# Performance work log

Measured on AMD Instinct MI355X. Metric: run time of the kernel, lower is better.

Reference implementation:

```python
import jax, jax.numpy as jnp
import numpy as np

N = 131072   # octree nodes at this depth
K = 27       # 3x3x3 kernel taps
CIN = 32
COUT = 32
EPS = 1e-5   # BatchNorm1d default eps


def setup_inputs() -> dict:
    key = jax.random.key(0)
    k1, k2, k3, k4, k5 = jax.random.split(key, 5)
    data = jax.random.normal(k1, (N, CIN), dtype=jnp.float32)
    # deconv weight: one [Cin, Cout] matrix per kernel tap
    weight = jax.random.normal(k2, (K, CIN, COUT), dtype=jnp.float32) * 0.05
    gamma = 1.0 + 0.1 * jax.random.normal(k3, (COUT,), dtype=jnp.float32)
    beta = 0.1 * jax.random.normal(k4, (COUT,), dtype=jnp.float32)
    # octree neighbor table: for each input node, the K output nodes it scatters into
    neigh = jax.random.randint(k5, (N, K), 0, N, dtype=jnp.int32)
    return {"data": data, "weight": weight, "gamma": gamma, "beta": beta, "neigh": neigh}


def reference(data, weight, gamma, beta, neigh):
    # Sparse transposed conv (stride=1): each node i produces a contribution
    # data[i] @ weight[k] that is scatter-added into output node neigh[i, k].
    contrib = jnp.einsum('ni,kio->nko', data, weight)          # [N, K, Cout]
    out = jax.ops.segment_sum(contrib.reshape(-1, COUT),
                              neigh.reshape(-1),
                              num_segments=N)                   # [N, Cout]
    # BatchNorm1d (training mode: batch statistics over the node dimension)
    mean = jnp.mean(out, axis=0)
    var = jnp.var(out, axis=0)
    y = gamma * (out - mean) * jax.lax.rsqrt(var + EPS) + beta
    # ReLU
    return jnp.maximum(y, 0.0)
```

## Files before the change

kernel.cpp:

```cpp
#include <hip/hip_runtime.h>
#include <hip/hip_bf16.h>
#include <hip/hip_fp16.h>

#define NN 131072
#define KK 27
#define CC 32
#define EPSV 1e-5f

#define WS_STATS 0
#define WS_WPERM 256
#define WS_ACC   65536
#define WS_NEEDED ((size_t)WS_ACC + (size_t)NN * CC * 2)

typedef __bf16 bf16x8 __attribute__((ext_vector_type(8)));
typedef short s16x8 __attribute__((ext_vector_type(8)));
typedef float f32x4 __attribute__((ext_vector_type(4)));

__device__ inline unsigned short f2bf(float f) {
    unsigned int u = __float_as_uint(f);
    u += 0x7FFF + ((u >> 16) & 1);
    return (unsigned short)(u >> 16);
}

__global__ __launch_bounds__(256) void prep_weights_kernel(
    const float* __restrict__ weight, unsigned short* __restrict__ wperm)
{
    const int p = blockIdx.x * 256 + threadIdx.x;
    if (p >= KK * 1024) return;
    const int k  = p >> 10;
    const int ci = (p >> 5) & 31;
    const int c  = p & 31;
    const unsigned short v = f2bf(weight[p]);
    const int chalf = c & 1;
    const int col   = c >> 1;
    const int fl = col | ((ci >> 3) << 4);
    const int j = ci & 7;
    wperm[(((k << 1) | chalf) * 64 + fl) * 8 + j] = v;
}

__global__ __launch_bounds__(256) void scatter_kernel(
    const float* __restrict__ data, const unsigned short* __restrict__ wperm,
    const int* __restrict__ neigh, __half2* __restrict__ acc2)
{
    const int tid = threadIdx.x;
    const int lane = tid & 63;
    const int wv = tid >> 6;
    const int node_base = blockIdx.x * 128 + wv * 32;

    const int quad = lane >> 4;
    const int m = lane & 15;
    const int rq = quad << 2;

    s16x8 afr[2];
    #pragma unroll
    for (int g = 0; g < 2; ++g) {
        const int node = node_base + g * 16 + m;
        const float* src = data + node * 32 + quad * 8;
        const float4 v0 = *(const float4*)(src);
        const float4 v1 = *(const float4*)(src + 4);
        s16x8 s;
        s[0] = (short)f2bf(v0.x); s[1] = (short)f2bf(v0.y);
        s[2] = (short)f2bf(v0.z); s[3] = (short)f2bf(v0.w);
        s[4] = (short)f2bf(v1.x); s[5] = (short)f2bf(v1.y);
        s[6] = (short)f2bf(v1.z); s[7] = (short)f2bf(v1.w);
        afr[g] = s;
    }

    const s16x8* wp = (const s16x8*)wperm;
    const f32x4 zero = {0.f, 0.f, 0.f, 0.f};

    int nj0[4], nj1[4];
    #pragma unroll
    for (int r = 0; r < 4; ++r) {
        nj0[r] = neigh[(node_base + rq + r) * KK];
        nj1[r] = neigh[(node_base + 16 + rq + r) * KK];
    }
    s16x8 bs0 = wp[lane];
    s16x8 bs1 = wp[64 + lane];

    for (int k = 0; k < KK; ++k) {
        const int kn = (k < KK - 1) ? k + 1 : k;
        int nn0[4], nn1[4];
        #pragma unroll
        for (int r = 0; r < 4; ++r) {
            nn0[r] = neigh[(node_base + rq + r) * KK + kn];
            nn1[r] = neigh[(node_base + 16 + rq + r) * KK + kn];
        }
        const s16x8 nbs0 = wp[(kn * 2) * 64 + lane];
        const s16x8 nbs1 = wp[(kn * 2 + 1) * 64 + lane];

        {
            const f32x4 d0 = __builtin_amdgcn_mfma_f32_16x16x32_bf16(
                __builtin_bit_cast(bf16x8, afr[0]), __builtin_bit_cast(bf16x8, bs0),
                zero, 0, 0, 0);
            const f32x4 d1 = __builtin_amdgcn_mfma_f32_16x16x32_bf16(
                __builtin_bit_cast(bf16x8, afr[0]), __builtin_bit_cast(bf16x8, bs1),
                zero, 0, 0, 0);
            #pragma unroll
            for (int r = 0; r < 4; ++r) {
                __half2 v;
                v.x = __float2half(d0[r]);
                v.y = __float2half(d1[r]);
                unsafeAtomicAdd(&acc2[nj0[r] * 16 + m], v);
            }
        }
        {
            const f32x4 d0 = __builtin_amdgcn_mfma_f32_16x16x32_bf16(
                __builtin_bit_cast(bf16x8, afr[1]), __builtin_bit_cast(bf16x8, bs0),
                zero, 0, 0, 0);
            const f32x4 d1 = __builtin_amdgcn_mfma_f32_16x16x32_bf16(
                __builtin_bit_cast(bf16x8, afr[1]), __builtin_bit_cast(bf16x8, bs1),
                zero, 0, 0, 0);
            #pragma unroll
            for (int r = 0; r < 4; ++r) {
                __half2 v;
                v.x = __float2half(d0[r]);
                v.y = __float2half(d1[r]);
                unsafeAtomicAdd(&acc2[nj1[r] * 16 + m], v);
            }
        }

        bs0 = nbs0; bs1 = nbs1;
        #pragma unroll
        for (int r = 0; r < 4; ++r) { nj0[r] = nn0[r]; nj1[r] = nn1[r]; }
    }
}

__global__ __launch_bounds__(256) void stats_kernel(
    const __half2* __restrict__ acc2, float* __restrict__ stats)
{
    __shared__ float ls[16][33], ls2[16][33];
    const int tid = threadIdx.x;
    const int c2 = tid & 15, rg = tid >> 4;
    float sx = 0.f, sy = 0.f, s2x = 0.f, s2y = 0.f;
    const int row0 = blockIdx.x * 512;
    for (int it = 0; it < 32; ++it) {
        const __half2 h = acc2[(row0 + it * 16 + rg) * 16 + c2];
        const float vx = __half2float(h.x), vy = __half2float(h.y);
        sx += vx; sy += vy; s2x += vx * vx; s2y += vy * vy;
    }
    ls[rg][2 * c2] = sx;  ls[rg][2 * c2 + 1] = sy;
    ls2[rg][2 * c2] = s2x; ls2[rg][2 * c2 + 1] = s2y;
    __syncthreads();
    if (tid < 32) {
        float S = 0.f, S2 = 0.f;
        #pragma unroll
        for (int g = 0; g < 16; ++g) { S += ls[g][tid]; S2 += ls2[g][tid]; }
        atomicAdd(&stats[tid], S);
        atomicAdd(&stats[32 + tid], S2);
    }
}

__global__ __launch_bounds__(256) void bn_relu_kernel(
    const __half2* __restrict__ acc2, float* __restrict__ out,
    const float* __restrict__ stats,
    const float* __restrict__ gamma, const float* __restrict__ beta)
{
    __shared__ float sc[32], sh[32];
    const int tid = threadIdx.x;
    if (tid < 32) {
        const float mean = stats[tid] * (1.0f / NN);
        const float var  = stats[32 + tid] * (1.0f / NN) - mean * mean;
        const float s = gamma[tid] * rsqrtf(var + EPSV);
        sc[tid] = s;
        sh[tid] = beta[tid] - mean * s;
    }
    __syncthreads();
    const int idx = blockIdx.x * 256 + tid;
    const int c0 = (idx & 3) << 3;
    const __half2 h4[4] = { acc2[idx * 4], acc2[idx * 4 + 1],
                            acc2[idx * 4 + 2], acc2[idx * 4 + 3] };
    float4 o0, o1;
    o0.x = fmaxf(__half2float(h4[0].x) * sc[c0]     + sh[c0],     0.f);
    o0.y = fmaxf(__half2float(h4[0].y) * sc[c0 + 1] + sh[c0 + 1], 0.f);
    o0.z = fmaxf(__half2float(h4[1].x) * sc[c0 + 2] + sh[c0 + 2], 0.f);
    o0.w = fmaxf(__half2float(h4[1].y) * sc[c0 + 3] + sh[c0 + 3], 0.f);
    o1.x = fmaxf(__half2float(h4[2].x) * sc[c0 + 4] + sh[c0 + 4], 0.f);
    o1.y = fmaxf(__half2float(h4[2].y) * sc[c0 + 5] + sh[c0 + 5], 0.f);
    o1.z = fmaxf(__half2float(h4[3].x) * sc[c0 + 6] + sh[c0 + 6], 0.f);
    o1.w = fmaxf(__half2float(h4[3].y) * sc[c0 + 7] + sh[c0 + 7], 0.f);
    ((float4*)out)[idx * 2]     = o0;
    ((float4*)out)[idx * 2 + 1] = o1;
}

__global__ __launch_bounds__(256) void scatter_f32_kernel(
    const float* __restrict__ data, const float* __restrict__ weight,
    const int* __restrict__ neigh, float* __restrict__ out)
{
    __shared__ unsigned short wfrag[KK * 2 * 64 * 8];
    const int tid = threadIdx.x;
    const int lane = tid & 63;
    const int wv = tid >> 6;
    const int node_base = blockIdx.x * 128;
    for (int p = tid; p < KK * 1024; p += 256) {
        const int k  = p >> 10;
        const int ci = (p >> 5) & 31;
        const int c  = p & 31;
        const unsigned short v = f2bf(weight[p]);
        const int chalf = c >> 4;
        const int fl = (c & 15) | ((ci >> 3) << 4);
        const int j = ci & 7;
        wfrag[(((k << 1) | chalf) * 64 + fl) * 8 + j] = v;
    }
    const int quad = lane >> 4;
    const int m = lane & 15;
    s16x8 afr[2];
    #pragma unroll
    for (int g = 0; g < 2; ++g) {
        const int node = node_base + wv * 32 + g * 16 + m;
        const float* src = data + node * 32 + quad * 8;
        const float4 v0 = *(const float4*)(src);
        const float4 v1 = *(const float4*)(src + 4);
        s16x8 s;
        s[0] = (short)f2bf(v0.x); s[1] = (short)f2bf(v0.y);
        s[2] = (short)f2bf(v0.z); s[3] = (short)f2bf(v0.w);
        s[4] = (short)f2bf(v1.x); s[5] = (short)f2bf(v1.y);
        s[6] = (short)f2bf(v1.z); s[7] = (short)f2bf(v1.w);
        afr[g] = s;
    }
    __syncthreads();
    const int rq = quad << 2;
    const f32x4 zero = {0.f, 0.f, 0.f, 0.f};
    for (int k = 0; k < KK; ++k) {
        int nj[2][4];
        #pragma unroll
        for (int g = 0; g < 2; ++g)
            #pragma unroll
            for (int r = 0; r < 4; ++r) {
                const int node = node_base + wv * 32 + g * 16 + rq + r;
                nj[g][r] = neigh[node * KK + k];
            }
        #pragma unroll
        for (int ch = 0; ch < 2; ++ch) {
            const s16x8 bs = *(const s16x8*)&wfrag[((((k << 1) | ch)) * 64 + lane) * 8];
            const bf16x8 bfr = __builtin_bit_cast(bf16x8, bs);
            const int c = (ch << 4) | m;
            #pragma unroll
            for (int g = 0; g < 2; ++g) {
                f32x4 a2 = __builtin_amdgcn_mfma_f32_16x16x32_bf16(
                    __builtin_bit_cast(bf16x8, afr[g]), bfr, zero, 0, 0, 0);
                #pragma unroll
                for (int r = 0; r < 4; ++r)
                    __hip_atomic_fetch_add(&out[nj[g][r] * 32 + c], a2[r],
                                           __ATOMIC_RELAXED, __HIP_MEMORY_SCOPE_AGENT);
            }
        }
    }
}

__global__ __launch_bounds__(256) void stats_f32_kernel(
    const float* __restrict__ out, float* __restrict__ stats)
{
    __shared__ float ls[256], ls2[256];
    const int tid = threadIdx.x;
    const int c = tid & 31, rg = tid >> 5;
    float s = 0.f, s2 = 0.f;
    const int row0 = blockIdx.x * 512;
    for (int it = 0; it < 64; ++it) {
        const float v = out[(row0 + it * 8 + rg) * 32 + c];
        s += v; s2 += v * v;
    }
    ls[tid] = s; ls2[tid] = s2;
    __syncthreads();
    if (tid < 32) {
        float S = 0.f, S2 = 0.f;
        #pragma unroll
        for (int r = 0; r < 8; ++r) { S += ls[r * 32 + tid]; S2 += ls2[r * 32 + tid]; }
        atomicAdd(&stats[tid], S);
        atomicAdd(&stats[32 + tid], S2);
    }
}

__global__ __launch_bounds__(256) void bn_relu_f32_kernel(
    float* __restrict__ out, const float* __restrict__ stats,
    const float* __restrict__ gamma, const float* __restrict__ beta)
{
    __shared__ float sc[32], sh[32];
    const int tid = threadIdx.x;
    if (tid < 32) {
        const float mean = stats[tid] * (1.0f / NN);
        const float var  = stats[32 + tid] * (1.0f / NN) - mean * mean;
        const float s = gamma[tid] * rsqrtf(var + EPSV);
        sc[tid] = s;
        sh[tid] = beta[tid] - mean * s;
    }
    __syncthreads();
    const int idx = blockIdx.x * 256 + tid;
    float4 v = ((float4*)out)[idx];
    const int cb = (idx & 7) << 2;
    v.x = fmaxf(v.x * sc[cb]     + sh[cb],     0.f);
    v.y = fmaxf(v.y * sc[cb + 1] + sh[cb + 1], 0.f);
    v.z = fmaxf(v.z * sc[cb + 2] + sh[cb + 2], 0.f);
    v.w = fmaxf(v.w * sc[cb + 3] + sh[cb + 3], 0.f);
    ((float4*)out)[idx] = v;
}

extern "C" void kernel_launch(void* const* d_in, const int* in_sizes, int n_in,
                              void* d_out, int out_size, void* d_ws, size_t ws_size,
                              hipStream_t stream) {
    const float* data   = (const float*)d_in[0];
    const float* weight = (const float*)d_in[1];
    const float* gamma  = (const float*)d_in[2];
    const float* beta   = (const float*)d_in[3];
    const int*   neigh  = (const int*)d_in[4];
    float* out = (float*)d_out;
    char* ws = (char*)d_ws;
    float* stats = (float*)(ws + WS_STATS);

    if (ws_size >= WS_NEEDED) {
        __half2* acc2 = (__half2*)(ws + WS_ACC);
        unsigned short* wperm = (unsigned short*)(ws + WS_WPERM);
        hipMemsetAsync(ws + WS_STATS, 0, 256, stream);
        hipMemsetAsync(ws + WS_ACC, 0, (size_t)NN * CC * 2, stream);
        prep_weights_kernel<<<(KK * 1024 + 255) / 256, 256, 0, stream>>>(weight, wperm);
        scatter_kernel<<<NN / 128, 256, 0, stream>>>(data, wperm, neigh, acc2);
        stats_kernel<<<NN / 512, 256, 0, stream>>>(acc2, stats);
        bn_relu_kernel<<<(NN * CC / 8) / 256, 256, 0, stream>>>(acc2, out, stats, gamma, beta);
    } else {
        hipMemsetAsync(out, 0, (size_t)NN * CC * sizeof(float), stream);
        hipMemsetAsync(stats, 0, 64 * sizeof(float), stream);
        scatter_f32_kernel<<<NN / 128, 256, 0, stream>>>(data, weight, neigh, out);
        stats_f32_kernel<<<NN / 512, 256, 0, stream>>>(out, stats);
        bn_relu_f32_kernel<<<(NN * CC / 4) / 256, 256, 0, stream>>>(out, stats, gamma, beta);
    }
}
```

Baseline: 271.4 us.

## Replace atomic scatter with bucketed inverse-index gather and fused BN statistics

Builds an inverse neighbour table by bucketing every (input node, tap) pair per output node with a counter, capped at 64 slots. Each output row then gathers fp16 input rows, pre-sums them per tap in LDS, and runs one fp16 MFMA chain over the 27 taps. The output is written once in fp32, and the batch-norm sums are reduced in the same kernel. This replaces tens of millions of half2 atomics on the output with a few million integer atomics on counters. In exchange it adds a pair-fill pass, fp16 accumulation of the per-tap sums, silent truncation of rows with more than 64 contributors, and a much larger workspace requirement.

Result: slower. 544.9 us (+100.8%).

```diff
diff --git a/kernel.cpp b/kernel.cpp
--- a/kernel.cpp
+++ b/kernel.cpp
@@ -7,12 +7,22 @@
 #define CC 32
 #define EPSV 1e-5f
 
-#define WS_STATS 0
-#define WS_WPERM 256
-#define WS_ACC   65536
-#define WS_NEEDED ((size_t)WS_ACC + (size_t)NN * CC * 2)
+#define WS_STATS   0
+#define WS_CNT     256
+#define WS_WPERM   (256 + 524288)
+#define WS_PAIRS   579840
+#define WS_DATA16  34134272
+#define WS_NEED_GATHER ((size_t)WS_DATA16 + (size_t)NN * CC * 2)
+
+#define T2_WPERM 256
+#define T2_ACC   65536
+#define WS_NEED_T2 ((size_t)T2_ACC + (size_t)NN * CC * 2)
+
+#define CAP  64
+#define XSTR 472
 
 typedef __bf16 bf16x8 __attribute__((ext_vector_type(8)));
+typedef _Float16 f16x8 __attribute__((ext_vector_type(8)));
 typedef short s16x8 __attribute__((ext_vector_type(8)));
 typedef float f32x4 __attribute__((ext_vector_type(4)));
 
@@ -21,8 +31,186 @@
     u += 0x7FFF + ((u >> 16) & 1);
     return (unsigned short)(u >> 16);
 }
-
-__global__ __launch_bounds__(256) void prep_weights_kernel(
+__device__ inline unsigned short f2h(float f) {
+    return __builtin_bit_cast(unsigned short, __float2half(f));
+}
+__device__ inline unsigned int h2add(unsigned int a, unsigned int b) {
+    __half2 x = __builtin_bit_cast(__half2, a);
+    __half2 y = __builtin_bit_cast(__half2, b);
+    return __builtin_bit_cast(unsigned int, __hadd2(x, y));
+}
+
+
+__global__ __launch_bounds__(256) void prep_kernel(
+    const float* __restrict__ data, const float* __restrict__ weight,
+    unsigned short* __restrict__ data16, unsigned short* __restrict__ wperm)
+{
+    const int b = blockIdx.x;
+    if (b < 2048) {
+        const int tg = b * 256 + threadIdx.x;
+        const float4 v0 = ((const float4*)data)[tg * 2];
+        const float4 v1 = ((const float4*)data)[tg * 2 + 1];
+        union { unsigned short us[8]; uint4 u4; } o;
+        o.us[0] = f2h(v0.x); o.us[1] = f2h(v0.y);
+        o.us[2] = f2h(v0.z); o.us[3] = f2h(v0.w);
+        o.us[4] = f2h(v1.x); o.us[5] = f2h(v1.y);
+        o.us[6] = f2h(v1.z); o.us[7] = f2h(v1.w);
+        ((uint4*)data16)[tg] = o.u4;
+    } else {
+        const int p = (b - 2048) * 256 + threadIdx.x;
+        const int k  = p >> 10;
+        const int ci = (p >> 5) & 31;
+        const int c  = p & 31;
+        const unsigned short v = f2h(weight[p]);
+        const int chalf = c & 1;
+        const int col   = c >> 1;
+        const int fl = col | ((ci >> 3) << 4);
+        const int j = ci & 7;
+        wperm[(((k << 1) | chalf) * 64 + fl) * 8 + j] = v;
+    }
+}
+
+__global__ __launch_bounds__(256) void fill_kernel(
+    const int* __restrict__ neigh, unsigned int* __restrict__ cnt,
+    unsigned int* __restrict__ pairs)
+{
+    const unsigned int p = blockIdx.x * 256 + threadIdx.x;
+    const unsigned int o = (unsigned int)neigh[p];
+    const unsigned int i = p / 27u;
+    const unsigned int k = p - i * 27u;
+    const unsigned int slot = atomicAdd(&cnt[o], 1u);
+    if (slot < CAP) pairs[(o << 6) | slot] = (i << 5) | k;
+}
+
+__global__ __launch_bounds__(256) void gather_kernel(
+    const unsigned short* __restrict__ data16,
+    const unsigned short* __restrict__ wperm,
+    const unsigned int* __restrict__ cnt, const unsigned int* __restrict__ pairs,
+    float* __restrict__ out, float* __restrict__ stats)
+{
+    __shared__ unsigned short Xs[4][16 * XSTR];
+    __shared__ float sarr[4][16][4];
+
+    const int tid = threadIdx.x;
+    const int lane = tid & 63;
+    const int wv = tid >> 6;
+    const int row0 = blockIdx.x * 64 + wv * 16;
+
+    const int rl  = lane >> 2;
+    const int seg = lane & 3;
+    const int row_g = row0 + rl;
+
+    const unsigned int cfull = cnt[row_g];
+    const int c = (int)(cfull < (unsigned)CAP ? cfull : (unsigned)CAP);
+    const int cm1 = c > 0 ? c - 1 : 0;
+    int maxc = c;
+    #pragma unroll
+    for (int off = 1; off < 64; off <<= 1) {
+        const int o2 = __shfl_xor(maxc, off);
+        maxc = maxc > o2 ? maxc : o2;
+    }
+
+    const unsigned int* prow = pairs + ((size_t)row_g << 6);
+
+    const int quad = lane >> 4;
+    const int m = lane & 15;
+    f32x4 acc0 = {0.f, 0.f, 0.f, 0.f}, acc1 = {0.f, 0.f, 0.f, 0.f};
+    const uint4* wq = (const uint4*)wperm;
+    const uint4* dq = (const uint4*)data16;
+    unsigned short* xw = &Xs[wv][0];
+
+    for (int g = 0; g < 2; ++g) {
+        const int k0 = g * 14;
+        const int NT = g ? 13 : 14;
+
+        {
+            const uint4 z = {0u, 0u, 0u, 0u};
+            #pragma unroll
+            for (int it = 0; it < 15; ++it) {
+                const int idx = lane + it * 64;
+                if (idx < (16 * XSTR) / 8) ((uint4*)xw)[idx] = z;
+            }
+        }
+
+        unsigned int p0 = prow[0];
+        unsigned int p1 = prow[1 < cm1 ? 1 : cm1];
+        unsigned int p2 = prow[2 < cm1 ? 2 : cm1];
+        unsigned int p3 = prow[3 < cm1 ? 3 : cm1];
+        uint4 d0 = {0,0,0,0}, d1 = {0,0,0,0};
+        {
+            const int kk = (int)(p0 & 31u) - k0;
+            if (kk >= 0 && kk < NT) d0 = dq[(((p0 >> 5) & (NN - 1)) << 2) | seg];
+        }
+        {
+            const int kk = (int)(p1 & 31u) - k0;
+            if (kk >= 0 && kk < NT) d1 = dq[(((p1 >> 5) & (NN - 1)) << 2) | seg];
+        }
+
+        for (int t = 0; t < maxc; ++t) {
+            const int tp = t + 4;
+            const unsigned int pn = prow[tp < cm1 ? tp : cm1];
+            uint4 dn = {0,0,0,0};
+            {
+                const int kk = (int)(p2 & 31u) - k0;
+                if (kk >= 0 && kk < NT) dn = dq[(((p2 >> 5) & (NN - 1)) << 2) | seg];
+            }
+            {
+                const int kk = (int)(p0 & 31u) - k0;
+                if (t < c && kk >= 0 && kk < NT) {
+                    uint4* xp = (uint4*)(xw + rl * XSTR + kk * 32 + seg * 8);
+                    uint4 cur = *xp;
+                    cur.x = h2add(cur.x, d0.x); cur.y = h2add(cur.y, d0.y);
+                    cur.z = h2add(cur.z, d0.z); cur.w = h2add(cur.w, d0.w);
+                    *xp = cur;
+                }
+            }
+            p0 = p1; p1 = p2; p2 = p3; p3 = pn;
+            d0 = d1; d1 = dn;
+        }
+
+        uint4 b0 = wq[(k0 * 2 + 0) * 64 + lane];
+        uint4 b1 = wq[(k0 * 2 + 1) * 64 + lane];
+        for (int kk = 0; kk < NT; ++kk) {
+            const int ktn = (kk + 1 < NT) ? (k0 + kk + 1) : (k0 + kk);
+            const uint4 nb0 = wq[(ktn * 2 + 0) * 64 + lane];
+            const uint4 nb1 = wq[(ktn * 2 + 1) * 64 + lane];
+            const uint4 av = *(const uint4*)(xw + m * XSTR + kk * 32 + quad * 8);
+            const f16x8 af = __builtin_bit_cast(f16x8, av);
+            acc0 = __builtin_amdgcn_mfma_f32_16x16x32_f16(
+                af, __builtin_bit_cast(f16x8, b0), acc0, 0, 0, 0);
+            acc1 = __builtin_amdgcn_mfma_f32_16x16x32_f16(
+                af, __builtin_bit_cast(f16x8, b1), acc1, 0, 0, 0);
+            b0 = nb0; b1 = nb1;
+        }
+    }
+
+    float s0 = 0.f, s1 = 0.f, q0 = 0.f, q1 = 0.f;
+    #pragma unroll
+    for (int r = 0; r < 4; ++r) {
+        const float a = acc0[r], b = acc1[r];
+        s0 += a; s1 += b; q0 += a * a; q1 += b * b;
+        float2 v; v.x = a; v.y = b;
+        *(float2*)(out + ((size_t)(row0 + quad * 4 + r)) * 32 + 2 * m) = v;
+    }
+    s0 += __shfl_xor(s0, 16); s0 += __shfl_xor(s0, 32);
+    s1 += __shfl_xor(s1, 16); s1 += __shfl_xor(s1, 32);
+    q0 += __shfl_xor(q0, 16); q0 += __shfl_xor(q0, 32);
+    q1 += __shfl_xor(q1, 16); q1 += __shfl_xor(q1, 32);
+    if (quad == 0) {
+        sarr[wv][m][0] = s0; sarr[wv][m][1] = s1;
+        sarr[wv][m][2] = q0; sarr[wv][m][3] = q1;
+    }
+    __syncthreads();
+    if (tid < 64) {
+        const int ch = tid & 31, isq = tid >> 5;
+        float v = 0.f;
+        #pragma unroll
+        for (int w = 0; w < 4; ++w) v += sarr[w][ch >> 1][(isq << 1) | (ch & 1)];
+        atomicAdd(&stats[isq * 32 + ch], v);
+    }
+}
+
+__global__ __launch_bounds__(256) void prep_weights_bf16_kernel(
     const float* __restrict__ weight, unsigned short* __restrict__ wperm)
 {
     const int p = blockIdx.x * 256 + threadIdx.x;
@@ -46,7 +234,6 @@
     const int lane = tid & 63;
     const int wv = tid >> 6;
     const int node_base = blockIdx.x * 128 + wv * 32;
-
     const int quad = lane >> 4;
     const int m = lane & 15;
     const int rq = quad << 2;
@@ -88,7 +275,6 @@
         }
         const s16x8 nbs0 = wp[(kn * 2) * 64 + lane];
         const s16x8 nbs1 = wp[(kn * 2 + 1) * 64 + lane];
-
         {
             const f32x4 d0 = __builtin_amdgcn_mfma_f32_16x16x32_bf16(
                 __builtin_bit_cast(bf16x8, afr[0]), __builtin_bit_cast(bf16x8, bs0),
@@ -119,7 +305,6 @@
                 unsafeAtomicAdd(&acc2[nj1[r] * 16 + m], v);
             }
         }
-
         bs0 = nbs0; bs1 = nbs1;
         #pragma unroll
         for (int r = 0; r < 4; ++r) { nj0[r] = nn0[r]; nj1[r] = nn1[r]; }
@@ -307,18 +492,28 @@
     char* ws = (char*)d_ws;
     float* stats = (float*)(ws + WS_STATS);
 
-    if (ws_size >= WS_NEEDED) {
-        __half2* acc2 = (__half2*)(ws + WS_ACC);
-        unsigned short* wperm = (unsigned short*)(ws + WS_WPERM);
+    if (ws_size >= WS_NEED_GATHER) {
+        unsigned int*   cnt    = (unsigned int*)(ws + WS_CNT);
+        unsigned short* wperm  = (unsigned short*)(ws + WS_WPERM);
+        unsigned int*   pairs  = (unsigned int*)(ws + WS_PAIRS);
+        unsigned short* data16 = (unsigned short*)(ws + WS_DATA16);
+        hipMemsetAsync(ws, 0, 256 + (size_t)NN * 4, stream);
+        prep_kernel<<<2156, 256, 0, stream>>>(data, weight, data16, wperm);
+        fill_kernel<<<(NN * KK) / 256, 256, 0, stream>>>(neigh, cnt, pairs);
+        gather_kernel<<<NN / 64, 256, 0, stream>>>(data16, wperm, cnt, pairs, out, stats);
+        bn_relu_f32_kernel<<<(NN * CC / 4) / 256, 256, 0, stream>>>(out, stats, gamma, beta);
+    } else if (ws_size >= WS_NEED_T2) {
+        __half2* acc2 = (__half2*)(ws + T2_ACC);
+        unsigned short* wperm = (unsigned short*)(ws + T2_WPERM);
         hipMemsetAsync(ws + WS_STATS, 0, 256, stream);
-        hipMemsetAsync(ws + WS_ACC, 0, (size_t)NN * CC * 2, stream);
-        prep_weights_kernel<<<(KK * 1024 + 255) / 256, 256, 0, stream>>>(weight, wperm);
+        hipMemsetAsync(ws + T2_ACC, 0, (size_t)NN * CC * 2, stream);
+        prep_weights_bf16_kernel<<<(KK * 1024 + 255) / 256, 256, 0, stream>>>(weight, wperm);
         scatter_kernel<<<NN / 128, 256, 0, stream>>>(data, wperm, neigh, acc2);
         stats_kernel<<<NN / 512, 256, 0, stream>>>(acc2, stats);
         bn_relu_kernel<<<(NN * CC / 8) / 256, 256, 0, stream>>>(acc2, out, stats, gamma, beta);
     } else {
         hipMemsetAsync(out, 0, (size_t)NN * CC * sizeof(float), stream);
-        hipMemsetAsync(stats, 0, 64 * sizeof(float), stream);
+        hipMemsetAsync(ws + WS_STATS, 0, 64 * sizeof(float), stream);
         scatter_f32_kernel<<<NN / 128, 256, 0, stream>>>(data, weight, neigh, out);
         stats_f32_kernel<<<NN / 512, 256, 0, stream>>>(out, stats);
         bn_relu_f32_kernel<<<(NN * CC / 4) / 256, 256, 0, stream>>>(out, stats, gamma, beta);
```

## Replace global atomic scatter with bin-sorted gather matmul and LDS accumulation

Applied to the files above, without the earlier changes.

Adds a new default path that turns the scatter into a gather. The (node, tap) records are partitioned into 512 bins by destination node, then counting-sorted by tap within each bin. A per-bin kernel runs fp16 MFMA on the gathered input rows and accumulates results with shared-memory float atomics. That kernel also writes fp32 outputs directly and fuses the BatchNorm statistics reduction. The aim is to remove the global fp16 atomics and the separate stats pass, at the cost of extra passes over the neighbor table. Bin capacity is fixed, so a skewed index distribution would silently drop contributions.

Result: slower. 729.7 us (+168.9%).

```diff
diff --git a/kernel.cpp b/kernel.cpp
--- a/kernel.cpp
+++ b/kernel.cpp
@@ -7,12 +7,24 @@
 #define CC 32
 #define EPSV 1e-5f
 
-#define WS_STATS 0
-#define WS_WPERM 256
-#define WS_ACC   65536
-#define WS_NEEDED ((size_t)WS_ACC + (size_t)NN * CC * 2)
+#define NBINS   512
+#define CAPBIN  7680
+#define CAPB    24
+#define WS_STATS   0
+#define WS_GCNT    256
+#define WS_KOFF    2304
+#define WS_WPERM   59648
+#define WS_RAW     114944
+#define WS_SORT    15843584
+#define WS_DATA16  31572224
+#define WS_NEED_GATHER ((size_t)WS_DATA16 + (size_t)NN * CC * 2)
+
+#define T2_WPERM 256
+#define T2_ACC   65536
+#define WS_NEED_T2 ((size_t)T2_ACC + (size_t)NN * CC * 2)
 
 typedef __bf16 bf16x8 __attribute__((ext_vector_type(8)));
+typedef _Float16 f16x8 __attribute__((ext_vector_type(8)));
 typedef short s16x8 __attribute__((ext_vector_type(8)));
 typedef float f32x4 __attribute__((ext_vector_type(4)));
 
@@ -21,8 +33,229 @@
     u += 0x7FFF + ((u >> 16) & 1);
     return (unsigned short)(u >> 16);
 }
-
-__global__ __launch_bounds__(256) void prep_weights_kernel(
+__device__ inline unsigned short f2h(float f) {
+    return __builtin_bit_cast(unsigned short, __float2half(f));
+}
+
+
+__global__ __launch_bounds__(256) void prep_kernel(
+    const float* __restrict__ data, const float* __restrict__ weight,
+    unsigned short* __restrict__ data16, unsigned short* __restrict__ wperm)
+{
+    const int b = blockIdx.x;
+    if (b < 2048) {
+        const int tg = b * 256 + threadIdx.x;
+        const float4 v0 = ((const float4*)data)[tg * 2];
+        const float4 v1 = ((const float4*)data)[tg * 2 + 1];
+        union { unsigned short us[8]; uint4 u4; } o;
+        o.us[0] = f2h(v0.x); o.us[1] = f2h(v0.y);
+        o.us[2] = f2h(v0.z); o.us[3] = f2h(v0.w);
+        o.us[4] = f2h(v1.x); o.us[5] = f2h(v1.y);
+        o.us[6] = f2h(v1.z); o.us[7] = f2h(v1.w);
+        ((uint4*)data16)[tg] = o.u4;
+    } else {
+        const int p = (b - 2048) * 256 + threadIdx.x;
+        const int k  = p >> 10;
+        const int ci = (p >> 5) & 31;
+        const int c  = p & 31;
+        const unsigned short v = f2h(weight[p]);
+        const int chalf = c & 1;
+        const int col   = c >> 1;
+        const int fl = col | ((ci >> 3) << 4);
+        const int j = ci & 7;
+        wperm[(((k << 1) | chalf) * 64 + fl) * 8 + j] = v;
+    }
+}
+
+__global__ __launch_bounds__(256) void partition_kernel(
+    const int* __restrict__ neigh, unsigned int* __restrict__ gcnt,
+    unsigned int* __restrict__ raw)
+{
+    __shared__ unsigned int lcnt[NBINS];
+    __shared__ unsigned int lbuf[NBINS * CAPB];
+    const int tid = threadIdx.x;
+    for (int t = tid; t < NBINS; t += 256) lcnt[t] = 0;
+    __syncthreads();
+    const int base = blockIdx.x * 4096;
+    #pragma unroll
+    for (int j = 0; j < 16; ++j) {
+        const int p = base + j * 256 + tid;
+        const unsigned int o = (unsigned int)neigh[p];
+        const unsigned int i = (unsigned int)p / 27u;
+        const unsigned int k = (unsigned int)p - i * 27u;
+        const unsigned int rec = (k << 25) | (i << 8) | (o & 255u);
+        const unsigned int bin = o >> 8;
+        const unsigned int slot = atomicAdd(&lcnt[bin], 1u);
+        if (slot < CAPB) {
+            lbuf[bin * CAPB + slot] = rec;
+        } else {
+            const unsigned int gp = atomicAdd(&gcnt[bin], 1u);
+            if (gp < CAPBIN) raw[(size_t)bin * CAPBIN + gp] = rec;
+        }
+    }
+    __syncthreads();
+    for (int b2 = tid; b2 < NBINS; b2 += 256) {
+        unsigned int nb = lcnt[b2]; if (nb > CAPB) nb = CAPB;
+        if (nb == 0) continue;
+        const unsigned int gbase = atomicAdd(&gcnt[b2], nb);
+        for (unsigned int s = 0; s < nb; ++s) {
+            const unsigned int gp = gbase + s;
+            if (gp < CAPBIN) raw[(size_t)b2 * CAPBIN + gp] = lbuf[b2 * CAPB + s];
+        }
+    }
+}
+
+__global__ __launch_bounds__(256) void binsort_kernel(
+    const unsigned int* __restrict__ gcnt, const unsigned int* __restrict__ raw,
+    unsigned int* __restrict__ sorted, unsigned int* __restrict__ koff)
+{
+    __shared__ unsigned int hist[28];
+    __shared__ unsigned int woffs[27];
+    const int b = blockIdx.x, tid = threadIdx.x;
+    if (tid < 28) hist[tid] = 0;
+    __syncthreads();
+    unsigned int n = gcnt[b]; if (n > CAPBIN) n = CAPBIN;
+    const unsigned int* rp = raw + (size_t)b * CAPBIN;
+    for (unsigned int t = tid; t < n; t += 256)
+        atomicAdd(&hist[rp[t] >> 25], 1u);
+    __syncthreads();
+    if (tid == 0) {
+        unsigned int run = 0;
+        for (int j = 0; j < 27; ++j) {
+            const unsigned int h = hist[j];
+            hist[j] = run; woffs[j] = run; run += h;
+        }
+        hist[27] = run;
+    }
+    __syncthreads();
+    if (tid < 28) koff[b * 28 + tid] = hist[tid];
+    unsigned int* sp = sorted + (size_t)b * CAPBIN;
+    for (unsigned int t = tid; t < n; t += 256) {
+        const unsigned int r = rp[t];
+        const unsigned int pos = atomicAdd(&woffs[r >> 25], 1u);
+        sp[pos] = r & 0x01FFFFFFu;
+    }
+}
+
+__global__ __launch_bounds__(256) void gathermm_kernel(
+    const unsigned short* __restrict__ data16,
+    const unsigned short* __restrict__ wperm,
+    const unsigned int* __restrict__ sorted,
+    const unsigned int* __restrict__ koff,
+    float* __restrict__ out, float* __restrict__ stats)
+{
+    __shared__ float accS[256 * 33];
+    __shared__ float ps[8][32], ps2[8][32];
+    const int tid = threadIdx.x;
+    const int lane = tid & 63, wv = tid >> 6;
+    const int b = blockIdx.x;
+
+    for (int t = tid; t < 256 * 33; t += 256) accS[t] = 0.f;
+    __syncthreads();
+
+    const int q = lane >> 4, m = lane & 15;
+    const uint4* wq = (const uint4*)wperm;
+    const uint4* dq = (const uint4*)data16;
+    const unsigned int* so = sorted + (size_t)b * CAPBIN;
+    const unsigned int* kb = koff + b * 28;
+    const f32x4 zero = {0.f, 0.f, 0.f, 0.f};
+
+    for (int k = wv; k < KK; k += 4) {
+        const int s0  = (int)kb[k];
+        const int len = (int)kb[k + 1] - s0;
+        if (len <= 0) continue;
+        const unsigned int* sp2 = so + s0;
+        const int last = len - 1;
+        const uint4 b0 = wq[(k * 2) * 64 + lane];
+        const uint4 b1 = wq[(k * 2 + 1) * 64 + lane];
+
+        unsigned int recA = sp2[m < last ? m : last];
+        uint4 avA = dq[((recA >> 8) << 2) | q];
+        const int i1 = 16 + m;
+        unsigned int recB = sp2[i1 < last ? i1 : last];
+
+        for (int t = 0; t < len; t += 16) {
+            const int i2 = t + 32 + m;
+            const unsigned int recC = sp2[i2 < last ? i2 : last];
+            const uint4 avB = dq[((recB >> 8) << 2) | q];
+
+            const f32x4 d0 = __builtin_amdgcn_mfma_f32_16x16x32_f16(
+                __builtin_bit_cast(f16x8, avA), __builtin_bit_cast(f16x8, b0),
+                zero, 0, 0, 0);
+            const f32x4 d1 = __builtin_amdgcn_mfma_f32_16x16x32_f16(
+                __builtin_bit_cast(f16x8, avA), __builtin_bit_cast(f16x8, b1),
+                zero, 0, 0, 0);
+            #pragma unroll
+            for (int r2 = 0; r2 < 4; ++r2) {
+                const int jr = t + 4 * q + r2;
+                if (jr < len) {
+                    const unsigned int rr = sp2[jr];
+                    const int o = (int)(rr & 255u);
+                    atomicAdd(&accS[o * 33 + 2 * m],     d0[r2]);
+                    atomicAdd(&accS[o * 33 + 2 * m + 1], d1[r2]);
+                }
+            }
+            avA = avB; recB = recC;
+        }
+    }
+    __syncthreads();
+
+    {
+        const int row = tid;
+        const float* ar = &accS[row * 33];
+        float4* op = (float4*)(out + ((size_t)(b * 256 + row)) * 32);
+        #pragma unroll
+        for (int c4 = 0; c4 < 8; ++c4) {
+            float4 v;
+            v.x = ar[c4 * 4]; v.y = ar[c4 * 4 + 1];
+            v.z = ar[c4 * 4 + 2]; v.w = ar[c4 * 4 + 3];
+            op[c4] = v;
+        }
+    }
+    {
+        const int cc = tid & 31, rg = tid >> 5;
+        float s = 0.f, s2 = 0.f;
+        for (int rr = rg; rr < 256; rr += 8) {
+            const float v = accS[rr * 33 + cc];
+            s += v; s2 += v * v;
+        }
+        ps[rg][cc] = s; ps2[rg][cc] = s2;
+        __syncthreads();
+        if (tid < 32) {
+            float S = 0.f, S2 = 0.f;
+            #pragma unroll
+            for (int g = 0; g < 8; ++g) { S += ps[g][tid]; S2 += ps2[g][tid]; }
+            atomicAdd(&stats[tid], S);
+            atomicAdd(&stats[32 + tid], S2);
+        }
+    }
+}
+
+__global__ __launch_bounds__(256) void bn_relu_f32_kernel(
+    float* __restrict__ out, const float* __restrict__ stats,
+    const float* __restrict__ gamma, const float* __restrict__ beta)
+{
+    __shared__ float sc[32], sh[32];
+    const int tid = threadIdx.x;
+    if (tid < 32) {
+        const float mean = stats[tid] * (1.0f / NN);
+        const float var  = stats[32 + tid] * (1.0f / NN) - mean * mean;
+        const float s = gamma[tid] * rsqrtf(var + EPSV);
+        sc[tid] = s;
+        sh[tid] = beta[tid] - mean * s;
+    }
+    __syncthreads();
+    const int idx = blockIdx.x * 256 + tid;
+    float4 v = ((float4*)out)[idx];
+    const int cb = (idx & 7) << 2;
+    v.x = fmaxf(v.x * sc[cb]     + sh[cb],     0.f);
+    v.y = fmaxf(v.y * sc[cb + 1] + sh[cb + 1], 0.f);
+    v.z = fmaxf(v.z * sc[cb + 2] + sh[cb + 2], 0.f);
+    v.w = fmaxf(v.w * sc[cb + 3] + sh[cb + 3], 0.f);
+    ((float4*)out)[idx] = v;
+}
+
+__global__ __launch_bounds__(256) void prep_weights_bf16_kernel(
     const float* __restrict__ weight, unsigned short* __restrict__ wperm)
 {
     const int p = blockIdx.x * 256 + threadIdx.x;
@@ -46,7 +279,6 @@
     const int lane = tid & 63;
     const int wv = tid >> 6;
     const int node_base = blockIdx.x * 128 + wv * 32;
-
     const int quad = lane >> 4;
     const int m = lane & 15;
     const int rq = quad << 2;
@@ -88,7 +320,6 @@
         }
         const s16x8 nbs0 = wp[(kn * 2) * 64 + lane];
         const s16x8 nbs1 = wp[(kn * 2 + 1) * 64 + lane];
-
         {
             const f32x4 d0 = __builtin_amdgcn_mfma_f32_16x16x32_bf16(
                 __builtin_bit_cast(bf16x8, afr[0]), __builtin_bit_cast(bf16x8, bs0),
@@ -119,7 +350,6 @@
                 unsafeAtomicAdd(&acc2[nj1[r] * 16 + m], v);
             }
         }
-
         bs0 = nbs0; bs1 = nbs1;
         #pragma unroll
         for (int r = 0; r < 4; ++r) { nj0[r] = nn0[r]; nj1[r] = nn1[r]; }
@@ -271,30 +501,6 @@
     }
 }
 
-__global__ __launch_bounds__(256) void bn_relu_f32_kernel(
-    float* __restrict__ out, const float* __restrict__ stats,
-    const float* __restrict__ gamma, const float* __restrict__ beta)
-{
-    __shared__ float sc[32], sh[32];
-    const int tid = threadIdx.x;
-    if (tid < 32) {
-        const float mean = stats[tid] * (1.0f / NN);
-        const float var  = stats[32 + tid] * (1.0f / NN) - mean * mean;
-        const float s = gamma[tid] * rsqrtf(var + EPSV);
-        sc[tid] = s;
-        sh[tid] = beta[tid] - mean * s;
-    }
-    __syncthreads();
-    const int idx = blockIdx.x * 256 + tid;
-    float4 v = ((float4*)out)[idx];
-    const int cb = (idx & 7) << 2;
-    v.x = fmaxf(v.x * sc[cb]     + sh[cb],     0.f);
-    v.y = fmaxf(v.y * sc[cb + 1] + sh[cb + 1], 0.f);
-    v.z = fmaxf(v.z * sc[cb + 2] + sh[cb + 2], 0.f);
-    v.w = fmaxf(v.w * sc[cb + 3] + sh[cb + 3], 0.f);
-    ((float4*)out)[idx] = v;
-}
-
 extern "C" void kernel_launch(void* const* d_in, const int* in_sizes, int n_in,
                               void* d_out, int out_size, void* d_ws, size_t ws_size,
                               hipStream_t stream) {
@@ -307,18 +513,31 @@
     char* ws = (char*)d_ws;
     float* stats = (float*)(ws + WS_STATS);
 
-    if (ws_size >= WS_NEEDED) {
-        __half2* acc2 = (__half2*)(ws + WS_ACC);
-        unsigned short* wperm = (unsigned short*)(ws + WS_WPERM);
+    if (ws_size >= WS_NEED_GATHER) {
+        unsigned int*   gcnt   = (unsigned int*)(ws + WS_GCNT);
+        unsigned int*   koff   = (unsigned int*)(ws + WS_KOFF);
+        unsigned short* wperm  = (unsigned short*)(ws + WS_WPERM);
+        unsigned int*   raw    = (unsigned int*)(ws + WS_RAW);
+        unsigned int*   sorted = (unsigned int*)(ws + WS_SORT);
+        unsigned short* data16 = (unsigned short*)(ws + WS_DATA16);
+        hipMemsetAsync(ws, 0, 2304, stream);
+        prep_kernel<<<2156, 256, 0, stream>>>(data, weight, data16, wperm);
+        partition_kernel<<<(NN * KK) / 4096, 256, 0, stream>>>(neigh, gcnt, raw);
+        binsort_kernel<<<NBINS, 256, 0, stream>>>(gcnt, raw, sorted, koff);
+        gathermm_kernel<<<NBINS, 256, 0, stream>>>(data16, wperm, sorted, koff, out, stats);
+        bn_relu_f32_kernel<<<(NN * CC / 4) / 256, 256, 0, stream>>>(out, stats, gamma, beta);
+    } else if (ws_size >= WS_NEED_T2) {
+        __half2* acc2 = (__half2*)(ws + T2_ACC);
+        unsigned short* wperm = (unsigned short*)(ws + T2_WPERM);
         hipMemsetAsync(ws + WS_STATS, 0, 256, stream);
-        hipMemsetAsync(ws + WS_ACC, 0, (size_t)NN * CC * 2, stream);
-        prep_weights_kernel<<<(KK * 1024 + 255) / 256, 256, 0, stream>>>(weight, wperm);
+        hipMemsetAsync(ws + T2_ACC, 0, (size_t)NN * CC * 2, stream);
+        prep_weights_bf16_kernel<<<(KK * 1024 + 255) / 256, 256, 0, stream>>>(weight, wperm);
         scatter_kernel<<<NN / 128, 256, 0, stream>>>(data, wperm, neigh, acc2);
         stats_kernel<<<NN / 512, 256, 0, stream>>>(acc2, stats);
         bn_relu_kernel<<<(NN * CC / 8) / 256, 256, 0, stream>>>(acc2, out, stats, gamma, beta);
     } else {
         hipMemsetAsync(out, 0, (size_t)NN * CC * sizeof(float), stream);
-        hipMemsetAsync(stats, 0, 64 * sizeof(float), stream);
+        hipMemsetAsync(ws + WS_STATS, 0, 64 * sizeof(float), stream);
         scatter_f32_kernel<<<NN / 128, 256, 0, stream>>>(data, weight, neigh, out);
         stats_f32_kernel<<<NN / 512, 256, 0, stream>>>(out, stats);
         bn_relu_f32_kernel<<<(NN * CC / 4) / 256, 256, 0, stream>>>(out, stats, gamma, beta);
```

## Fuse weight prep, scatter, stats and BN-ReLU into one cooperative kernel

Applied to the files above, without the earlier changes.

Replaces the four separate launches (weight prep, scatter, stats, BN+ReLU) with one cooperative kernel of 512 blocks x 512 threads that uses grid-wide syncs between phases. The two memsets are merged into one by moving the accumulator directly after the stats area. The intent is to remove launch gaps and kernel-boundary drains. In exchange, every phase now runs on a fixed 512-block grid, which lowers occupancy and parallelism in the atomic-heavy scatter phase and adds three grid barriers. If the cooperative launch fails, it falls back to the old multi-kernel path.

New measurement: 426.6 us. +57.2%, slower.

```diff
diff --git a/kernel.cpp b/kernel.cpp
--- a/kernel.cpp
+++ b/kernel.cpp
@@ -1,6 +1,9 @@
 #include <hip/hip_runtime.h>
+#include <hip/hip_cooperative_groups.h>
 #include <hip/hip_bf16.h>
 #include <hip/hip_fp16.h>
+
+namespace cg = cooperative_groups;
 
 #define NN 131072
 #define KK 27
@@ -8,9 +11,9 @@
 #define EPSV 1e-5f
 
 #define WS_STATS 0
-#define WS_WPERM 256
-#define WS_ACC   65536
-#define WS_NEEDED ((size_t)WS_ACC + (size_t)NN * CC * 2)
+#define WS_ACC   512
+#define WS_WPERM (512 + (size_t)NN * CC * 2)
+#define WS_NEEDED (WS_WPERM + 55296)
 
 typedef __bf16 bf16x8 __attribute__((ext_vector_type(8)));
 typedef short s16x8 __attribute__((ext_vector_type(8)));
@@ -22,31 +25,11 @@
     return (unsigned short)(u >> 16);
 }
 
-__global__ __launch_bounds__(256) void prep_weights_kernel(
-    const float* __restrict__ weight, unsigned short* __restrict__ wperm)
-{
-    const int p = blockIdx.x * 256 + threadIdx.x;
-    if (p >= KK * 1024) return;
-    const int k  = p >> 10;
-    const int ci = (p >> 5) & 31;
-    const int c  = p & 31;
-    const unsigned short v = f2bf(weight[p]);
-    const int chalf = c & 1;
-    const int col   = c >> 1;
-    const int fl = col | ((ci >> 3) << 4);
-    const int j = ci & 7;
-    wperm[(((k << 1) | chalf) * 64 + fl) * 8 + j] = v;
-}
-
-__global__ __launch_bounds__(256) void scatter_kernel(
+__device__ inline void scatter_body(
     const float* __restrict__ data, const unsigned short* __restrict__ wperm,
-    const int* __restrict__ neigh, __half2* __restrict__ acc2)
-{
-    const int tid = threadIdx.x;
-    const int lane = tid & 63;
-    const int wv = tid >> 6;
-    const int node_base = blockIdx.x * 128 + wv * 32;
-
+    const int* __restrict__ neigh, __half2* __restrict__ acc2,
+    int node_base, int lane)
+{
     const int quad = lane >> 4;
     const int m = lane & 15;
     const int rq = quad << 2;
@@ -88,7 +71,6 @@
         }
         const s16x8 nbs0 = wp[(kn * 2) * 64 + lane];
         const s16x8 nbs1 = wp[(kn * 2 + 1) * 64 + lane];
-
         {
             const f32x4 d0 = __builtin_amdgcn_mfma_f32_16x16x32_bf16(
                 __builtin_bit_cast(bf16x8, afr[0]), __builtin_bit_cast(bf16x8, bs0),
@@ -119,11 +101,128 @@
                 unsafeAtomicAdd(&acc2[nj1[r] * 16 + m], v);
             }
         }
-
         bs0 = nbs0; bs1 = nbs1;
         #pragma unroll
         for (int r = 0; r < 4; ++r) { nj0[r] = nn0[r]; nj1[r] = nn1[r]; }
     }
+}
+
+__global__ __launch_bounds__(512, 4) void fused_kernel(
+    const float* __restrict__ data, const float* __restrict__ weight,
+    const float* __restrict__ gamma, const float* __restrict__ beta,
+    const int* __restrict__ neigh, unsigned short* __restrict__ wperm,
+    __half2* __restrict__ acc2, float* __restrict__ stats,
+    float* __restrict__ out)
+{
+    cg::grid_group grid = cg::this_grid();
+    const int tid = threadIdx.x;
+    const int bb = blockIdx.x;
+
+    __shared__ float psum[16][32], psq[16][32];
+    __shared__ float sc[32], sh[32];
+
+    {
+        const int p = bb * 512 + tid;
+        if (p < KK * 1024) {
+            const int k  = p >> 10;
+            const int ci = (p >> 5) & 31;
+            const int c  = p & 31;
+            const unsigned short v = f2bf(weight[p]);
+            const int chalf = c & 1;
+            const int col   = c >> 1;
+            const int fl = col | ((ci >> 3) << 4);
+            const int j = ci & 7;
+            wperm[(((k << 1) | chalf) * 64 + fl) * 8 + j] = v;
+        }
+    }
+    grid.sync();
+
+    {
+        const int lane = tid & 63, wv = tid >> 6;
+        scatter_body(data, wperm, neigh, acc2, bb * 256 + wv * 32, lane);
+    }
+    grid.sync();
+
+    {
+        const int c = tid & 31, rg = tid >> 5;
+        float s = 0.f, s2 = 0.f;
+        #pragma unroll
+        for (int i = 0; i < 16; ++i) {
+            const int row = bb * 256 + rg + 16 * i;
+            const __half2 h = acc2[row * 16 + (c >> 1)];
+            const float v = __half2float((c & 1) ? __high2half(h) : __low2half(h));
+            s += v; s2 += v * v;
+        }
+        psum[rg][c] = s; psq[rg][c] = s2;
+        __syncthreads();
+        if (tid < 32) {
+            float S = 0.f, S2 = 0.f;
+            #pragma unroll
+            for (int g = 0; g < 16; ++g) { S += psum[g][tid]; S2 += psq[g][tid]; }
+            atomicAdd(&stats[tid], S);
+            atomicAdd(&stats[32 + tid], S2);
+        }
+    }
+    grid.sync();
+
+    {
+        if (tid < 32) {
+            const float mean = stats[tid] * (1.0f / NN);
+            const float var  = stats[32 + tid] * (1.0f / NN) - mean * mean;
+            const float s = gamma[tid] * rsqrtf(var + EPSV);
+            sc[tid] = s;
+            sh[tid] = beta[tid] - mean * s;
+        }
+        __syncthreads();
+        const int row = bb * 256 + (tid >> 1);
+        const int half = tid & 1;
+        const __half2* ap = acc2 + row * 16 + half * 8;
+        const int c0 = half * 16;
+        float4 o0, o1, o2, o3;
+        o0.x = fmaxf(__half2float(ap[0].x) * sc[c0]      + sh[c0],      0.f);
+        o0.y = fmaxf(__half2float(ap[0].y) * sc[c0 + 1]  + sh[c0 + 1],  0.f);
+        o0.z = fmaxf(__half2float(ap[1].x) * sc[c0 + 2]  + sh[c0 + 2],  0.f);
+        o0.w = fmaxf(__half2float(ap[1].y) * sc[c0 + 3]  + sh[c0 + 3],  0.f);
+        o1.x = fmaxf(__half2float(ap[2].x) * sc[c0 + 4]  + sh[c0 + 4],  0.f);
+        o1.y = fmaxf(__half2float(ap[2].y) * sc[c0 + 5]  + sh[c0 + 5],  0.f);
+        o1.z = fmaxf(__half2float(ap[3].x) * sc[c0 + 6]  + sh[c0 + 6],  0.f);
+        o1.w = fmaxf(__half2float(ap[3].y) * sc[c0 + 7]  + sh[c0 + 7],  0.f);
+        o2.x = fmaxf(__half2float(ap[4].x) * sc[c0 + 8]  + sh[c0 + 8],  0.f);
+        o2.y = fmaxf(__half2float(ap[4].y) * sc[c0 + 9]  + sh[c0 + 9],  0.f);
+        o2.z = fmaxf(__half2float(ap[5].x) * sc[c0 + 10] + sh[c0 + 10], 0.f);
+        o2.w = fmaxf(__half2float(ap[5].y) * sc[c0 + 11] + sh[c0 + 11], 0.f);
+        o3.x = fmaxf(__half2float(ap[6].x) * sc[c0 + 12] + sh[c0 + 12], 0.f);
+        o3.y = fmaxf(__half2float(ap[6].y) * sc[c0 + 13] + sh[c0 + 13], 0.f);
+        o3.z = fmaxf(__half2float(ap[7].x) * sc[c0 + 14] + sh[c0 + 14], 0.f);
+        o3.w = fmaxf(__half2float(ap[7].y) * sc[c0 + 15] + sh[c0 + 15], 0.f);
+        float4* op = (float4*)(out + (size_t)row * 32 + c0);
+        op[0] = o0; op[1] = o1; op[2] = o2; op[3] = o3;
+    }
+}
+
+__global__ __launch_bounds__(256) void prep_weights_bf16_kernel(
+    const float* __restrict__ weight, unsigned short* __restrict__ wperm)
+{
+    const int p = blockIdx.x * 256 + threadIdx.x;
+    if (p >= KK * 1024) return;
+    const int k  = p >> 10;
+    const int ci = (p >> 5) & 31;
+    const int c  = p & 31;
+    const unsigned short v = f2bf(weight[p]);
+    const int chalf = c & 1;
+    const int col   = c >> 1;
+    const int fl = col | ((ci >> 3) << 4);
+    const int j = ci & 7;
+    wperm[(((k << 1) | chalf) * 64 + fl) * 8 + j] = v;
+}
+
+__global__ __launch_bounds__(256) void scatter_kernel(
+    const float* __restrict__ data, const unsigned short* __restrict__ wperm,
+    const int* __restrict__ neigh, __half2* __restrict__ acc2)
+{
+    const int tid = threadIdx.x;
+    scatter_body(data, wperm, neigh, acc2,
+                 blockIdx.x * 128 + (tid >> 6) * 32, tid & 63);
 }
 
 __global__ __launch_bounds__(256) void stats_kernel(
@@ -310,15 +409,23 @@
     if (ws_size >= WS_NEEDED) {
         __half2* acc2 = (__half2*)(ws + WS_ACC);
         unsigned short* wperm = (unsigned short*)(ws + WS_WPERM);
-        hipMemsetAsync(ws + WS_STATS, 0, 256, stream);
-        hipMemsetAsync(ws + WS_ACC, 0, (size_t)NN * CC * 2, stream);
-        prep_weights_kernel<<<(KK * 1024 + 255) / 256, 256, 0, stream>>>(weight, wperm);
-        scatter_kernel<<<NN / 128, 256, 0, stream>>>(data, wperm, neigh, acc2);
-        stats_kernel<<<NN / 512, 256, 0, stream>>>(acc2, stats);
-        bn_relu_kernel<<<(NN * CC / 8) / 256, 256, 0, stream>>>(acc2, out, stats, gamma, beta);
+        hipMemsetAsync(ws, 0, WS_ACC + (size_t)NN * CC * 2, stream);
+
+        void* args[] = { (void*)&data, (void*)&weight, (void*)&gamma,
+                         (void*)&beta, (void*)&neigh, (void*)&wperm,
+                         (void*)&acc2, (void*)&stats, (void*)&out };
+        hipError_t rc = hipLaunchCooperativeKernel(
+            (const void*)fused_kernel, dim3(512), dim3(512), args, 0, stream);
+
+        if (rc != hipSuccess) {
+            prep_weights_bf16_kernel<<<(KK * 1024 + 255) / 256, 256, 0, stream>>>(weight, wperm);
+            scatter_kernel<<<NN / 128, 256, 0, stream>>>(data, wperm, neigh, acc2);
+            stats_kernel<<<NN / 512, 256, 0, stream>>>(acc2, stats);
+            bn_relu_kernel<<<(NN * CC / 8) / 256, 256, 0, stream>>>(acc2, out, stats, gamma, beta);
+        }
     } else {
         hipMemsetAsync(out, 0, (size_t)NN * CC * sizeof(float), stream);
-        hipMemsetAsync(stats, 0, 64 * sizeof(float), stream);
+        hipMemsetAsync(ws + WS_STATS, 0, 64 * sizeof(float), stream);
         scatter_f32_kernel<<<NN / 128, 256, 0, stream>>>(data, weight, neigh, out);
         stats_f32_kernel<<<NN / 512, 256, 0, stream>>>(out, stats);
         bn_relu_f32_kernel<<<(NN * CC / 4) / 256, 256, 0, stream>>>(out, stats, gamma, beta);
```
